# Performance work log

Measured on AMD Instinct MI355X. Metric: run time of the kernel, lower is better.

Reference implementation:

```python
import jax, jax.numpy as jnp
import numpy as np

B, N, D2, S = 64, 4096, 128, 512  # b, n, 2*d, size_s


def setup_inputs() -> dict:
    key = jax.random.key(0)
    k1, k2, k3, k4 = jax.random.split(key, 4)
    s_past = jax.random.randint(k1, (B, N), 0, S)
    yq = jax.random.normal(k2, (B, 1, D2), dtype=jnp.float32)
    y_past = jax.random.normal(k3, (B, N, D2), dtype=jnp.float32)
    w_mat = jax.random.normal(k4, (D2, D2), dtype=jnp.float32)
    return {"s_past": s_past, "yq": yq, "y_past": y_past, "w_mat": w_mat, "size_s": S}


def reference(s_past, yq, y_past, w_mat, size_s):
    # attn_logits[b,n] = yq[b,0,:] @ w_mat @ y_past[b,n,:]
    attn_logits = jnp.einsum('bqd,de,bne->bn', yq, w_mat, y_past)
    attn = jax.nn.softmax(attn_logits, axis=-1)  # (b, n)
    b, n = s_past.shape
    # post_est[b, s] = sum_n attn[b, n] * [s_past[b, n] == s]
    # fused scatter-add instead of materializing one-hot (b, n, S)
    flat_ids = (s_past + size_s * jnp.arange(b, dtype=s_past.dtype)[:, None]).reshape(-1)
    post_est = jax.ops.segment_sum(attn.reshape(-1), flat_ids,
                                   num_segments=b * size_s).reshape(b, size_s)
    return post_est
```

## Files before the change

kernel.cpp:

```cpp
#include <hip/hip_runtime.h>
#include <math.h>

#define BB 64
#define NN 4096
#define DD 128
#define SS 512
#define CHUNKS 16
#define ROWS_PER_CHUNK 256
#define SUBT 4

__global__ void compute_q_kernel(const float* __restrict__ yq,
                                 const float* __restrict__ w,
                                 float* __restrict__ q) {
    int b = blockIdx.x;
    int e = threadIdx.x;
    __shared__ float syq[DD];
    syq[e] = yq[b * DD + e];
    __syncthreads();
    float acc = 0.f;
#pragma unroll
    for (int d = 0; d < DD; ++d) acc = fmaf(syq[d], w[d * DD + e], acc);
    q[b * DD + e] = acc;
}

__global__ __launch_bounds__(256) void logits_kernel(
    const float* __restrict__ y_past, const float* __restrict__ q,
    float* __restrict__ logits, float* __restrict__ pmax,
    float* __restrict__ psum) {
    int b = blockIdx.x, chunk = blockIdx.y;
    int t = threadIdx.x;

    __shared__ float4 ytile[64 * 33];
    __shared__ float4 qsh4[32];
    __shared__ float wred[8];

    if (t < 32) qsh4[t] = ((const float4*)(q + b * DD))[t];
    __syncthreads();

    int j = t & 3;
    int r = t >> 2;
    float4 qreg[8];
#pragma unroll
    for (int k = 0; k < 8; ++k) qreg[k] = qsh4[j * 8 + k];

    const float4* gp =
        (const float4*)y_past + ((size_t)b * NN + (size_t)chunk * ROWS_PER_CHUNK) * 32;

    float pv[SUBT];
#pragma unroll
    for (int s = 0; s < SUBT; ++s) {
#pragma unroll
        for (int k = 0; k < 8; ++k) {
            int idx = t + k * 256;
            int rr = idx >> 5, cc = idx & 31;
            ytile[rr * 33 + cc] = gp[s * 2048 + idx];
        }
        __syncthreads();

        float4 acc = {0.f, 0.f, 0.f, 0.f};
#pragma unroll
        for (int k = 0; k < 8; ++k) {
            float4 yv = ytile[r * 33 + j * 8 + k];
            acc.x = fmaf(qreg[k].x, yv.x, acc.x);
            acc.y = fmaf(qreg[k].y, yv.y, acc.y);
            acc.z = fmaf(qreg[k].z, yv.z, acc.z);
            acc.w = fmaf(qreg[k].w, yv.w, acc.w);
        }
        float p = (acc.x + acc.y) + (acc.z + acc.w);
        p += __shfl_xor(p, 1, 64);
        p += __shfl_xor(p, 2, 64);
        if (j == 0)
            logits[(size_t)b * NN + chunk * ROWS_PER_CHUNK + s * 64 + r] = p;
        pv[s] = p;
        __syncthreads();
    }

    float m = fmaxf(fmaxf(pv[0], pv[1]), fmaxf(pv[2], pv[3]));
#pragma unroll
    for (int off = 32; off > 0; off >>= 1) m = fmaxf(m, __shfl_xor(m, off, 64));
    int wave = t >> 6, lane = t & 63;
    if (lane == 0) wred[wave] = m;
    __syncthreads();
    m = fmaxf(fmaxf(wred[0], wred[1]), fmaxf(wred[2], wred[3]));

    float ls = __expf(pv[0] - m) + __expf(pv[1] - m) + __expf(pv[2] - m) +
               __expf(pv[3] - m);
#pragma unroll
    for (int off = 32; off > 0; off >>= 1) ls += __shfl_xor(ls, off, 64);
    if (lane == 0) wred[4 + wave] = ls;
    __syncthreads();
    if (t == 0) {
        pmax[b * CHUNKS + chunk] = m;
        psum[b * CHUNKS + chunk] =
            (wred[4] + wred[5] + wred[6] + wred[7]) * 0.25f;
    }
}

__global__ __launch_bounds__(1024) void scatter_kernel(
    const float* __restrict__ logits, const float* __restrict__ pmax,
    const float* __restrict__ psum, const int* __restrict__ s_past,
    float* __restrict__ out) {
    int b = blockIdx.x;
    int t = threadIdx.x;
    __shared__ float bins[SS];
    __shared__ float cm[CHUNKS], cs[CHUNKS];
    __shared__ float sM, sInv;

    if (t < CHUNKS) {
        cm[t] = pmax[b * CHUNKS + t];
        cs[t] = psum[b * CHUNKS + t];
    }
    if (t < SS) bins[t] = 0.f;
    __syncthreads();
    if (t == 0) {
        float M = cm[0];
#pragma unroll
        for (int i = 1; i < CHUNKS; ++i) M = fmaxf(M, cm[i]);
        float S = 0.f;
#pragma unroll
        for (int i = 0; i < CHUNKS; ++i) S += cs[i] * __expf(cm[i] - M);
        sM = M;
        sInv = 1.f / S;
    }
    __syncthreads();

    float M = sM, inv = sInv;
    float4 lg = ((const float4*)(logits + (size_t)b * NN))[t];
    int4 sp = ((const int4*)(s_past + (size_t)b * NN))[t];
    atomicAdd(&bins[sp.x], __expf(lg.x - M) * inv);
    atomicAdd(&bins[sp.y], __expf(lg.y - M) * inv);
    atomicAdd(&bins[sp.z], __expf(lg.z - M) * inv);
    atomicAdd(&bins[sp.w], __expf(lg.w - M) * inv);
    __syncthreads();
    if (t < SS) out[b * SS + t] = bins[t];
}

extern "C" void kernel_launch(void* const* d_in, const int* in_sizes, int n_in,
                              void* d_out, int out_size, void* d_ws, size_t ws_size,
                              hipStream_t stream) {
    const int*   s_past = (const int*)d_in[0];
    const float* yq     = (const float*)d_in[1];
    const float* y_past = (const float*)d_in[2];
    const float* w_mat  = (const float*)d_in[3];

    float* ws     = (float*)d_ws;
    float* q      = ws;
    float* logits = q + BB * DD;
    float* pmax   = logits + BB * NN;
    float* psum   = pmax + BB * CHUNKS;
    float* out    = (float*)d_out;

    compute_q_kernel<<<BB, DD, 0, stream>>>(yq, w_mat, q);
    logits_kernel<<<dim3(BB, CHUNKS), 256, 0, stream>>>(y_past, q, logits,
                                                        pmax, psum);
    scatter_kernel<<<BB, 1024, 0, stream>>>(logits, pmax, psum, s_past, out);
}
```

Baseline: 211.8 us.

## Fuse q projection and per-chunk histogram into logits kernel, combine partial bins

Folds the q = yq·W projection into each logits block, so every chunk block recomputes q from W, and removes the separate q kernel. Each chunk now scatters its exp(logit - chunk_max) values into a shared-memory histogram and writes per-chunk bins. A small combine kernel rescales those bins by each chunk max, normalises and writes the output. This drops one launch and the logits round trip. In exchange W is read redundantly 1024 times and the block gains a 128-step serial dot-product phase.

```diff
diff --git a/kernel.cpp b/kernel.cpp
--- a/kernel.cpp
+++ b/kernel.cpp
@@ -6,45 +6,45 @@
 #define DD 128
 #define SS 512
 #define CHUNKS 16
-#define ROWS_PER_CHUNK 256
+#define RPC 256
 #define SUBT 4
 
-__global__ void compute_q_kernel(const float* __restrict__ yq,
-                                 const float* __restrict__ w,
-                                 float* __restrict__ q) {
-    int b = blockIdx.x;
-    int e = threadIdx.x;
-    __shared__ float syq[DD];
-    syq[e] = yq[b * DD + e];
-    __syncthreads();
-    float acc = 0.f;
-#pragma unroll
-    for (int d = 0; d < DD; ++d) acc = fmaf(syq[d], w[d * DD + e], acc);
-    q[b * DD + e] = acc;
-}
-
-__global__ __launch_bounds__(256) void logits_kernel(
-    const float* __restrict__ y_past, const float* __restrict__ q,
-    float* __restrict__ logits, float* __restrict__ pmax,
-    float* __restrict__ psum) {
+__global__ __launch_bounds__(256) void fused_kernel(
+    const float* __restrict__ y_past, const float* __restrict__ yq,
+    const float* __restrict__ w, const int* __restrict__ s_past,
+    float* __restrict__ bins_g, float* __restrict__ pmax) {
     int b = blockIdx.x, chunk = blockIdx.y;
     int t = threadIdx.x;
 
     __shared__ float4 ytile[64 * 33];
-    __shared__ float4 qsh4[32];
+    __shared__ float syq[DD];
+    __shared__ float qsh[DD];
+    __shared__ float bins[SS];
+    __shared__ int   ssh[RPC];
     __shared__ float wred[8];
 
-    if (t < 32) qsh4[t] = ((const float4*)(q + b * DD))[t];
+    if (t < DD) syq[t] = yq[b * DD + t];
+    bins[t] = 0.f;
+    bins[t + 256] = 0.f;
+    ssh[t] = s_past[b * NN + chunk * RPC + t];
+    __syncthreads();
+
+    if (t < DD) {
+        float acc = 0.f;
+#pragma unroll
+        for (int d = 0; d < DD; ++d) acc = fmaf(syq[d], w[d * DD + t], acc);
+        qsh[t] = acc;
+    }
     __syncthreads();
 
     int j = t & 3;
     int r = t >> 2;
     float4 qreg[8];
 #pragma unroll
-    for (int k = 0; k < 8; ++k) qreg[k] = qsh4[j * 8 + k];
+    for (int k = 0; k < 8; ++k) qreg[k] = ((const float4*)qsh)[j * 8 + k];
 
     const float4* gp =
-        (const float4*)y_past + ((size_t)b * NN + (size_t)chunk * ROWS_PER_CHUNK) * 32;
+        (const float4*)y_past + ((size_t)b * NN + (size_t)chunk * RPC) * 32;
 
     float pv[SUBT];
 #pragma unroll
@@ -69,8 +69,6 @@
         float p = (acc.x + acc.y) + (acc.z + acc.w);
         p += __shfl_xor(p, 1, 64);
         p += __shfl_xor(p, 2, 64);
-        if (j == 0)
-            logits[(size_t)b * NN + chunk * ROWS_PER_CHUNK + s * 64 + r] = p;
         pv[s] = p;
         __syncthreads();
     }
@@ -83,56 +81,58 @@
     __syncthreads();
     m = fmaxf(fmaxf(wred[0], wred[1]), fmaxf(wred[2], wred[3]));
 
-    float ls = __expf(pv[0] - m) + __expf(pv[1] - m) + __expf(pv[2] - m) +
-               __expf(pv[3] - m);
+    if (j == 0) {
 #pragma unroll
-    for (int off = 32; off > 0; off >>= 1) ls += __shfl_xor(ls, off, 64);
-    if (lane == 0) wred[4 + wave] = ls;
+        for (int s = 0; s < SUBT; ++s)
+            atomicAdd(&bins[ssh[s * 64 + r]], __expf(pv[s] - m));
+    }
     __syncthreads();
-    if (t == 0) {
-        pmax[b * CHUNKS + chunk] = m;
-        psum[b * CHUNKS + chunk] =
-            (wred[4] + wred[5] + wred[6] + wred[7]) * 0.25f;
-    }
+
+    float* bg = bins_g + ((size_t)b * CHUNKS + chunk) * SS;
+    bg[t] = bins[t];
+    bg[t + 256] = bins[t + 256];
+    if (t == 0) pmax[b * CHUNKS + chunk] = m;
 }
 
-__global__ __launch_bounds__(1024) void scatter_kernel(
-    const float* __restrict__ logits, const float* __restrict__ pmax,
-    const float* __restrict__ psum, const int* __restrict__ s_past,
+__global__ __launch_bounds__(512) void combine_kernel(
+    const float* __restrict__ bins_g, const float* __restrict__ pmax,
     float* __restrict__ out) {
     int b = blockIdx.x;
     int t = threadIdx.x;
-    __shared__ float bins[SS];
-    __shared__ float cm[CHUNKS], cs[CHUNKS];
-    __shared__ float sM, sInv;
+    __shared__ float scale[CHUNKS];
+    __shared__ float red[8];
+    __shared__ float sInv;
 
-    if (t < CHUNKS) {
-        cm[t] = pmax[b * CHUNKS + t];
-        cs[t] = psum[b * CHUNKS + t];
-    }
-    if (t < SS) bins[t] = 0.f;
+    if (t < CHUNKS) scale[t] = pmax[b * CHUNKS + t];
     __syncthreads();
     if (t == 0) {
-        float M = cm[0];
+        float M = scale[0];
 #pragma unroll
-        for (int i = 1; i < CHUNKS; ++i) M = fmaxf(M, cm[i]);
+        for (int c = 1; c < CHUNKS; ++c) M = fmaxf(M, scale[c]);
+#pragma unroll
+        for (int c = 0; c < CHUNKS; ++c) scale[c] = __expf(scale[c] - M);
+    }
+    __syncthreads();
+
+    float acc = 0.f;
+#pragma unroll
+    for (int c = 0; c < CHUNKS; ++c)
+        acc = fmaf(bins_g[((size_t)b * CHUNKS + c) * SS + t], scale[c], acc);
+
+    float s = acc;
+#pragma unroll
+    for (int off = 32; off > 0; off >>= 1) s += __shfl_xor(s, off, 64);
+    if ((t & 63) == 0) red[t >> 6] = s;
+    __syncthreads();
+    if (t == 0) {
         float S = 0.f;
 #pragma unroll
-        for (int i = 0; i < CHUNKS; ++i) S += cs[i] * __expf(cm[i] - M);
-        sM = M;
+        for (int i = 0; i < 8; ++i) S += red[i];
         sInv = 1.f / S;
     }
     __syncthreads();
 
-    float M = sM, inv = sInv;
-    float4 lg = ((const float4*)(logits + (size_t)b * NN))[t];
-    int4 sp = ((const int4*)(s_past + (size_t)b * NN))[t];
-    atomicAdd(&bins[sp.x], __expf(lg.x - M) * inv);
-    atomicAdd(&bins[sp.y], __expf(lg.y - M) * inv);
-    atomicAdd(&bins[sp.z], __expf(lg.z - M) * inv);
-    atomicAdd(&bins[sp.w], __expf(lg.w - M) * inv);
-    __syncthreads();
-    if (t < SS) out[b * SS + t] = bins[t];
+    out[b * SS + t] = acc * sInv;
 }
 
 extern "C" void kernel_launch(void* const* d_in, const int* in_sizes, int n_in,
@@ -144,14 +144,11 @@
     const float* w_mat  = (const float*)d_in[3];
 
     float* ws     = (float*)d_ws;
-    float* q      = ws;
-    float* logits = q + BB * DD;
-    float* pmax   = logits + BB * NN;
-    float* psum   = pmax + BB * CHUNKS;
+    float* bins_g = ws;
+    float* pmax   = bins_g + BB * CHUNKS * SS;
     float* out    = (float*)d_out;
 
-    compute_q_kernel<<<BB, DD, 0, stream>>>(yq, w_mat, q);
-    logits_kernel<<<dim3(BB, CHUNKS), 256, 0, stream>>>(y_past, q, logits,
-                                                        pmax, psum);
-    scatter_kernel<<<BB, 1024, 0, stream>>>(logits, pmax, psum, s_past, out);
+    fused_kernel<<<dim3(BB, CHUNKS), 256, 0, stream>>>(y_past, yq, w_mat,
+                                                       s_past, bins_g, pmax);
+    combine_kernel<<<BB, SS, 0, stream>>>(bins_g, pmax, out);
 }
```

New measurement: 204.9 us. -3.3%, faster.
